# Kernel tuning notes

Hardware: AMD Instinct MI355X
Metric: run time of the kernel (lower is better)

The kernel has to match this reference:

```python
import jax, jax.numpy as jnp
import numpy as np
import math

N, E = 8192, 32768
MUL_S, MUL_V = 32, 16          # 32x0e + 16x1o
DIM = MUL_S + 3 * MUL_V        # 80
NUM_RBF, HID = 16, 64
CUTOFF = 5.0
ALPHA = 5.0 / CUTOFF
# per-edge TP weight sizes (uvw paths): ss->s, s sh1->v, v sh0->v, vv->s, vv->v
O1 = MUL_S * MUL_S              # 1024
O2 = O1 + MUL_S * MUL_V         # 1536
O3 = O2 + MUL_V * MUL_V         # 1792
O4 = O3 + MUL_V * MUL_S         # 2304
WNUM = O4 + MUL_V * MUL_V       # 2560


def setup_inputs() -> dict:
    key = jax.random.key(0)
    ks = jax.random.split(key, 8)
    h = jax.random.normal(ks[0], (N, DIM), jnp.float32)
    pos = jax.random.normal(ks[1], (N, 3), jnp.float32)
    edge_index = jax.random.randint(ks[2], (2, E), 0, N)
    start = math.exp(-CUTOFF)
    means = jnp.linspace(start, 1.0, NUM_RBF).astype(jnp.float32)
    betas = jnp.full((NUM_RBF,), (2.0 / NUM_RBF * (1.0 - start)) ** -2, jnp.float32)
    W1 = jax.random.normal(ks[3], (NUM_RBF, HID), jnp.float32) / np.sqrt(NUM_RBF).astype(np.float32)
    b1 = jnp.zeros((HID,), jnp.float32)
    W2 = jax.random.normal(ks[4], (HID, WNUM), jnp.float32) / np.sqrt(HID).astype(np.float32)
    b2 = jnp.zeros((WNUM,), jnp.float32)
    Wss = jax.random.normal(ks[5], (MUL_S, MUL_S), jnp.float32)
    Wvv = jax.random.normal(ks[6], (MUL_V, MUL_V), jnp.float32)
    return {"h": h, "pos": pos, "edge_index": edge_index, "means": means,
            "betas": betas, "W1": W1, "b1": b1, "W2": W2, "b2": b2,
            "Wss": Wss, "Wvv": Wvv}


def reference(h, pos, edge_index, means, betas, W1, b1, W2, b2, Wss, Wvv):
    src, dst = edge_index[0], edge_index[1]
    vec = pos[dst] - pos[src]                           # [E,3]
    d = jnp.sqrt(jnp.sum(vec * vec, -1) + 1e-12)        # [E]
    y1 = math.sqrt(3.0) * vec / d[:, None]              # l=1 SH, component norm
    # ExpNormalSmearing with cosine cutoff
    cut = 0.5 * (jnp.cos(d * math.pi / CUTOFF) + 1.0) * (d < CUTOFF).astype(h.dtype)
    expd = jnp.exp(-ALPHA * d)[:, None]
    rbf = jnp.exp(-betas * (expd - means) ** 2) * cut[:, None]   # [E,NUM_RBF]
    # edge MLP -> per-edge TP weights
    ew = jax.nn.silu(rbf @ W1 + b1) @ W2 + b2            # [E,WNUM]
    w_ss = ew[:, :O1].reshape(E, MUL_S, MUL_S)
    w_sv = ew[:, O1:O2].reshape(E, MUL_S, MUL_V)
    w_vs = ew[:, O2:O3].reshape(E, MUL_V, MUL_V)
    w_vv0 = ew[:, O3:O4].reshape(E, MUL_V, MUL_S)
    w_vv1 = ew[:, O4:].reshape(E, MUL_V, MUL_V)
    hs = h[:, :MUL_S]                                    # [N,32]
    hv = h[:, MUL_S:].reshape(N, MUL_V, 3)               # [N,16,3]
    s_src = hs[src]                                      # [E,32]
    v_src = hv[src]                                      # [E,16,3]
    # scalar outputs: (0e x 0e -> 0e) + (1o x 1o -> 0e)
    p1 = jnp.einsum('eu,euw->ew', s_src, w_ss)
    dot = jnp.einsum('eud,ed->eu', v_src, y1) / math.sqrt(3.0)
    p4 = jnp.einsum('eu,euw->ew', dot, w_vv0)
    out_s = (p1 / math.sqrt(MUL_S) + p4 / math.sqrt(MUL_V)) / math.sqrt(2.0)
    # vector outputs: (0e x 1o -> 1o) + (1o x 0e -> 1o) + (1o x 1o -> 1o)
    p2 = jnp.einsum('eu,euw,ed->ewd', s_src, w_sv, y1)
    p3 = jnp.einsum('eud,euw->ewd', v_src, w_vs)
    cross = jnp.cross(v_src, y1[:, None, :]) / math.sqrt(2.0)
    p5 = jnp.einsum('eud,euw->ewd', cross, w_vv1)
    out_v = (p2 / math.sqrt(MUL_S) + p3 / math.sqrt(MUL_V) + p5 / math.sqrt(MUL_V)) / math.sqrt(3.0)
    msgs = jnp.concatenate([out_s, out_v.reshape(E, 3 * MUL_V)], -1)   # [E,80]
    # scatter-mean to destination nodes
    agg = jax.ops.segment_sum(msgs, dst, num_segments=N)
    cnt = jax.ops.segment_sum(jnp.ones((E,), msgs.dtype), dst, num_segments=N)
    agg = agg / jnp.maximum(cnt, 1.0)[:, None]
    # equivariant self-interaction (per-irrep channel mixing)
    si_s = hs @ Wss / math.sqrt(MUL_S)
    si_v = jnp.einsum('nud,uw->nwd', hv, Wvv) / math.sqrt(MUL_V)
    self_i = jnp.concatenate([si_s, si_v.reshape(N, 3 * MUL_V)], -1)
    return agg + self_i + h   # residual
```

## Files before the change

kernel.cpp:

```cpp
#include <hip/hip_runtime.h>
#include <math.h>

#define NN 8192
#define EE 32768
#define WN 2560
#define EW_STRIDE 260
#define HID_STRIDE 72

typedef unsigned short u16;
typedef unsigned int u32;
typedef short short8 __attribute__((ext_vector_type(8)));
typedef float f32x4 __attribute__((ext_vector_type(4)));

__device__ __forceinline__ u16 f2b(float f) {
    u32 x = __float_as_uint(f);
    return (u16)((x + 0x7fffu + ((x >> 16) & 1u)) >> 16);
}

__global__ __launch_bounds__(256) void w2_transpose(const float* __restrict__ W2,
                                                    u16* __restrict__ W2T) {
    __shared__ float tile[64][65];
    const int c0 = blockIdx.x << 6;
    const int t = threadIdx.x;
    const int tl = t & 63, th = t >> 6;
    #pragma unroll
    for (int r = 0; r < 16; ++r) {
        int k = (r << 2) + th;
        tile[k][tl] = W2[k * WN + c0 + tl];
    }
    __syncthreads();
    #pragma unroll
    for (int r = 0; r < 16; ++r) {
        int c = (r << 2) + th;
        W2T[(size_t)(c0 + c) * 64 + tl] = f2b(tile[tl][c]);
    }
}

__global__ __launch_bounds__(256, 2) void edge_kernel(
    const float* __restrict__ h, const float* __restrict__ pos, const int* __restrict__ ei,
    const float* __restrict__ means, const float* __restrict__ betas,
    const float* __restrict__ W1, const float* __restrict__ b1,
    const u16* __restrict__ W2T, const float* __restrict__ b2,
    float* __restrict__ agg, float* __restrict__ cnt)
{
    __shared__ alignas(16) u16 sh_hidb[32 * HID_STRIDE];
    __shared__ float sh_s[32][32];
    __shared__ float sh_dot[32][16];
    __shared__ float sh_v[32][48];
    __shared__ float sh_cross[32][48];
    __shared__ float sh_y1[32][3];
    __shared__ float sh_geo[32][2];
    __shared__ float sh_q2[32][16];
    __shared__ int   sh_src[32];
    __shared__ int   sh_dst[32];
    __shared__ float sh_ew[32 * EW_STRIDE];

    const int t = threadIdx.x;

    if (t < 32) {
        const int eg = (blockIdx.x << 5) + t;
        const int si = ei[eg];
        const int di = ei[EE + eg];
        float ax = pos[si*3+0], ay = pos[si*3+1], az = pos[si*3+2];
        float bx = pos[di*3+0], by = pos[di*3+1], bz = pos[di*3+2];
        float vx = bx-ax, vy = by-ay, vz = bz-az;
        float d = sqrtf(vx*vx + vy*vy + vz*vz + 1e-12f);
        float invd = 1.7320508075688772f / d;
        sh_y1[t][0] = vx*invd; sh_y1[t][1] = vy*invd; sh_y1[t][2] = vz*invd;
        sh_geo[t][0] = expf(-d);
        sh_geo[t][1] = (d < 5.0f) ? 0.5f*(cosf(d*0.6283185307179586f) + 1.0f) : 0.0f;
        sh_src[t] = si; sh_dst[t] = di;
    }
    __syncthreads();

    {
        const int e = t >> 3, r = t & 7;
        const float expd = sh_geo[e][0], cut = sh_geo[e][1];
        float rbf[16];
        #pragma unroll
        for (int k = 0; k < 16; ++k) {
            float td = expd - means[k];
            rbf[k] = expf(-betas[k]*td*td) * cut;
        }
        short8 pk;
        #pragma unroll
        for (int jj = 0; jj < 8; ++jj) {
            int j = (r << 3) + jj;
            float a = b1[j];
            #pragma unroll
            for (int k = 0; k < 16; ++k) a += rbf[k] * W1[(k<<6) + j];
            float s = a / (1.0f + expf(-a));
            pk[jj] = (short)f2b(s);
        }
        *(short8*)&sh_hidb[e*HID_STRIDE + (r<<3)] = pk;

        const int srcn = sh_src[e];
        const float* hrow = h + srcn*80;
        const float y1x = sh_y1[e][0], y1y = sh_y1[e][1], y1z = sh_y1[e][2];
        #pragma unroll
        for (int i = 0; i < 4; ++i) { int u = (r<<2)+i; sh_s[e][u] = hrow[u]; }
        #pragma unroll
        for (int i = 0; i < 2; ++i) {
            int u = (r<<1)+i;
            float v0 = hrow[32+u*3+0];
            float v1 = hrow[32+u*3+1];
            float v2 = hrow[32+u*3+2];
            sh_v[e][u*3+0] = v0; sh_v[e][u*3+1] = v1; sh_v[e][u*3+2] = v2;
            sh_dot[e][u] = (v0*y1x + v1*y1y + v2*y1z) * 0.5773502691896258f;
            sh_cross[e][u*3+0] = (v1*y1z - v2*y1y) * 0.7071067811865476f;
            sh_cross[e][u*3+1] = (v2*y1x - v0*y1z) * 0.7071067811865476f;
            sh_cross[e][u*3+2] = (v0*y1y - v1*y1x) * 0.7071067811865476f;
        }
    }
    __syncthreads();

    const int ln = t & 63, wv = t >> 6;
    const int quad = ln >> 4, lm = ln & 15;
    short8 af[2][2];
    #pragma unroll
    for (int mt = 0; mt < 2; ++mt)
        #pragma unroll
        for (int ks = 0; ks < 2; ++ks)
            af[mt][ks] = *(const short8*)&sh_hidb[(mt*16+lm)*HID_STRIDE + (ks<<5) + (quad<<3)];

    float outs[4] = {0.f,0.f,0.f,0.f};
    float q2r[2]  = {0.f,0.f};
    float outv[6] = {0.f,0.f,0.f,0.f,0.f,0.f};

    for (int ci = 0; ci < 10; ++ci) {
        if (ci) __syncthreads();

        short8 bf[4][2];
        float b2v[4];
        #pragma unroll
        for (int i = 0; i < 4; ++i) {
            const int coll = (((wv<<2)+i)<<4) + lm;
            const int col  = (ci<<8) + coll;
            #pragma unroll
            for (int ks = 0; ks < 2; ++ks)
                bf[i][ks] = *(const short8*)(W2T + (size_t)col*64 + (ks<<5) + (quad<<3));
            b2v[i] = b2[col];
        }
        f32x4 d[4][2];
        #pragma unroll
        for (int i = 0; i < 4; ++i) {
            d[i][0] = (f32x4){0.f,0.f,0.f,0.f};
            d[i][1] = (f32x4){0.f,0.f,0.f,0.f};
            d[i][0] = __builtin_amdgcn_mfma_f32_16x16x32_bf16(af[0][0], bf[i][0], d[i][0], 0,0,0);
            d[i][0] = __builtin_amdgcn_mfma_f32_16x16x32_bf16(af[0][1], bf[i][1], d[i][0], 0,0,0);
            d[i][1] = __builtin_amdgcn_mfma_f32_16x16x32_bf16(af[1][0], bf[i][0], d[i][1], 0,0,0);
            d[i][1] = __builtin_amdgcn_mfma_f32_16x16x32_bf16(af[1][1], bf[i][1], d[i][1], 0,0,0);
        }
        #pragma unroll
        for (int i = 0; i < 4; ++i) {
            const int coll = (((wv<<2)+i)<<4) + lm;
            #pragma unroll
            for (int r = 0; r < 4; ++r) {
                sh_ew[((quad<<2)+r)*EW_STRIDE + coll]    = d[i][0][r] + b2v[i];
                sh_ew[((quad<<2)+r+16)*EW_STRIDE + coll] = d[i][1][r] + b2v[i];
            }
        }
        __syncthreads();

        if (ci < 4) {
            const int ub = ci << 3;
            #pragma unroll
            for (int k = 0; k < 4; ++k) {
                int p = t + (k<<8); int e = p >> 5; int w = p & 31;
                float s = 0.f;
                #pragma unroll
                for (int j = 0; j < 8; ++j) s += sh_s[e][ub+j] * sh_ew[e*EW_STRIDE + (j<<5)+w];
                outs[k] += 0.125f * s;
            }
        } else if (ci < 6) {
            const int ub = (ci-4) << 4;
            #pragma unroll
            for (int k = 0; k < 2; ++k) {
                int q = t + (k<<8); int e = q >> 4; int w = q & 15;
                float s = 0.f;
                #pragma unroll
                for (int j = 0; j < 16; ++j) s += sh_s[e][ub+j] * sh_ew[e*EW_STRIDE + (j<<4)+w];
                q2r[k] += s;
            }
            if (ci == 5) {
                #pragma unroll
                for (int k = 0; k < 2; ++k) { int q = t + (k<<8); sh_q2[q>>4][q&15] = q2r[k]; }
            }
        } else if (ci == 6) {
            #pragma unroll
            for (int k = 0; k < 6; ++k) {
                int p = t + (k<<8); int e = p/48; int m = p - e*48; int w = m/3; int d2 = m - w*3;
                float s = 0.f;
                #pragma unroll
                for (int u = 0; u < 16; ++u) s += sh_v[e][u*3+d2] * sh_ew[e*EW_STRIDE + (u<<4)+w];
                outv[k] += 0.14433756729740643f * s;
            }
        } else if (ci < 9) {
            const int ub = (ci-7) << 3;
            #pragma unroll
            for (int k = 0; k < 4; ++k) {
                int p = t + (k<<8); int e = p >> 5; int w = p & 31;
                float s = 0.f;
                #pragma unroll
                for (int j = 0; j < 8; ++j) s += sh_dot[e][ub+j] * sh_ew[e*EW_STRIDE + (j<<5)+w];
                outs[k] += 0.17677669529663687f * s;
            }
        } else {
            #pragma unroll
            for (int k = 0; k < 6; ++k) {
                int p = t + (k<<8); int e = p/48; int m = p - e*48; int w = m/3; int d2 = m - w*3;
                float s = 0.f;
                #pragma unroll
                for (int u = 0; u < 16; ++u) s += sh_cross[e][u*3+d2] * sh_ew[e*EW_STRIDE + (u<<4)+w];
                outv[k] += 0.14433756729740643f * s;
            }
        }
    }

    #pragma unroll
    for (int k = 0; k < 4; ++k) {
        int p = t + (k<<8); int e = p >> 5; int w = p & 31;
        atomicAdd(&agg[sh_dst[e]*80 + w], outs[k]);
    }
    #pragma unroll
    for (int k = 0; k < 6; ++k) {
        int p = t + (k<<8); int e = p/48; int m = p - e*48; int w = m/3; int d2 = m - w*3;
        float val = outv[k] + sh_q2[e][w]*sh_y1[e][d2]*0.10206207261596574f;
        atomicAdd(&agg[sh_dst[e]*80 + 32 + m], val);
    }
    if (t < 32) atomicAdd(&cnt[sh_dst[t]], 1.0f);
}

__global__ __launch_bounds__(256, 4) void node_kernel(
    const float* __restrict__ h, const float* __restrict__ Wss, const float* __restrict__ Wvv,
    const float* __restrict__ agg, const float* __restrict__ cnt,
    float* __restrict__ out)
{
    const int idx = blockIdx.x*256 + threadIdx.x;
    const int n = idx / 80;
    const int j = idx - n*80;
    float a = agg[idx] / fmaxf(cnt[n], 1.0f);
    const float* hrow = h + n*80;
    float si = 0.f;
    if (j < 32) {
        #pragma unroll
        for (int u = 0; u < 32; ++u) si += hrow[u] * Wss[(u<<5)+j];
        si *= 0.17677669529663687f;
    } else {
        int m = j - 32; int w = m/3; int d = m - w*3;
        #pragma unroll
        for (int u = 0; u < 16; ++u) si += hrow[32+u*3+d] * Wvv[(u<<4)+w];
        si *= 0.25f;
    }
    out[idx] = a + si + hrow[j];
}

extern "C" void kernel_launch(void* const* d_in, const int* in_sizes, int n_in,
                              void* d_out, int out_size, void* d_ws, size_t ws_size,
                              hipStream_t stream) {
    const float* h     = (const float*)d_in[0];
    const float* pos   = (const float*)d_in[1];
    const int*   ei    = (const int*)d_in[2];
    const float* means = (const float*)d_in[3];
    const float* betas = (const float*)d_in[4];
    const float* W1    = (const float*)d_in[5];
    const float* b1    = (const float*)d_in[6];
    const float* W2    = (const float*)d_in[7];
    const float* b2    = (const float*)d_in[8];
    const float* Wss   = (const float*)d_in[9];
    const float* Wvv   = (const float*)d_in[10];

    float* agg = (float*)d_ws;
    float* cnt = agg + (size_t)NN*80;
    u16*   W2T = (u16*)(cnt + NN);

    hipMemsetAsync(d_ws, 0, (size_t)(NN*80 + NN)*sizeof(float), stream);
    hipLaunchKernelGGL(w2_transpose, dim3(WN/64), dim3(256), 0, stream, W2, W2T);
    hipLaunchKernelGGL(edge_kernel, dim3(EE/32), dim3(256), 0, stream,
                       h, pos, ei, means, betas, W1, b1, W2T, b2, agg, cnt);
    hipLaunchKernelGGL(node_kernel, dim3((NN*80)/256), dim3(256), 0, stream,
                       h, Wss, Wvv, agg, cnt, (float*)d_out);
}
```

Measured before the change: 155.6 us.

## Consume MFMA edge-weight outputs in registers and fold memset into prep kernel

The edge MLP output tile is no longer written to a large shared-memory buffer and re-read for each tensor-product path. Each wave now contracts its MFMA accumulator fragments directly against pre-scaled source features and keeps per-lane partial sums in registers. The partial sums from the four waves are reduced through shared memory once at the end. The per-chunk barriers go away and shared memory shrinks, which could allow more resident blocks. The workspace memset and the W2 transpose are also merged into a single prep kernel to save one launch. In exchange the kernel has a larger register footprint, a cross-wave reduction step, and scaling constants that were reworked and need to stay correct.

```diff
diff --git a/kernel.cpp b/kernel.cpp
--- a/kernel.cpp
+++ b/kernel.cpp
@@ -4,7 +4,6 @@
 #define NN 8192
 #define EE 32768
 #define WN 2560
-#define EW_STRIDE 260
 #define HID_STRIDE 72
 
 typedef unsigned short u16;
@@ -17,22 +16,31 @@
     return (u16)((x + 0x7fffu + ((x >> 16) & 1u)) >> 16);
 }
 
-__global__ __launch_bounds__(256) void w2_transpose(const float* __restrict__ W2,
-                                                    u16* __restrict__ W2T) {
-    __shared__ float tile[64][65];
-    const int c0 = blockIdx.x << 6;
-    const int t = threadIdx.x;
-    const int tl = t & 63, th = t >> 6;
-    #pragma unroll
-    for (int r = 0; r < 16; ++r) {
-        int k = (r << 2) + th;
-        tile[k][tl] = W2[k * WN + c0 + tl];
-    }
-    __syncthreads();
-    #pragma unroll
-    for (int r = 0; r < 16; ++r) {
-        int c = (r << 2) + th;
-        W2T[(size_t)(c0 + c) * 64 + tl] = f2b(tile[tl][c]);
+__global__ __launch_bounds__(256) void prep(const float* __restrict__ W2,
+                                            u16* __restrict__ W2T,
+                                            float* __restrict__ zbase) {
+    const int t = threadIdx.x, b = blockIdx.x;
+    const float4 z4 = {0.f, 0.f, 0.f, 0.f};
+    #pragma unroll
+    for (int k = 0; k < 3; ++k) {
+        int i = b * 768 + k * 256 + t;
+        if (i < 165888) ((float4*)zbase)[i] = z4;
+    }
+    if (b < 40) {
+        __shared__ float tile[64][65];
+        const int c0 = b << 6;
+        const int tl = t & 63, th = t >> 6;
+        #pragma unroll
+        for (int r = 0; r < 16; ++r) {
+            int kk = (r << 2) + th;
+            tile[kk][tl] = W2[kk * WN + c0 + tl];
+        }
+        __syncthreads();
+        #pragma unroll
+        for (int r = 0; r < 16; ++r) {
+            int c = (r << 2) + th;
+            W2T[(size_t)(c0 + c) * 64 + tl] = f2b(tile[tl][c]);
+        }
     }
 }
 
@@ -43,17 +51,20 @@
     const u16* __restrict__ W2T, const float* __restrict__ b2,
     float* __restrict__ agg, float* __restrict__ cnt)
 {
-    __shared__ alignas(16) u16 sh_hidb[32 * HID_STRIDE];
-    __shared__ float sh_s[32][32];
-    __shared__ float sh_dot[32][16];
-    __shared__ float sh_v[32][48];
-    __shared__ float sh_cross[32][48];
+    __shared__ alignas(16) char sbuf[50688];
+    float (*sh_ss)[33]    = (float (*)[33])(sbuf);
+    float (*sh_dot)[17]   = (float (*)[17])(sbuf + 4224);
+    float (*sh_v)[68]     = (float (*)[68])(sbuf + 6400);
+    float (*sh_cross)[68] = (float (*)[68])(sbuf + 15104);
+    u16*  sh_hidb         = (u16*)(sbuf + 23808);
+    float (*redS)[32][33] = (float (*)[32][33])(sbuf);
+    float (*redQ)[32][17] = (float (*)[32][17])(sbuf + 16896);
+    float (*redV)[32][49] = (float (*)[32][49])(sbuf + 25600);
+
     __shared__ float sh_y1[32][3];
     __shared__ float sh_geo[32][2];
-    __shared__ float sh_q2[32][16];
     __shared__ int   sh_src[32];
     __shared__ int   sh_dst[32];
-    __shared__ float sh_ew[32 * EW_STRIDE];
 
     const int t = threadIdx.x;
 
@@ -98,18 +109,20 @@
         const float* hrow = h + srcn*80;
         const float y1x = sh_y1[e][0], y1y = sh_y1[e][1], y1z = sh_y1[e][2];
         #pragma unroll
-        for (int i = 0; i < 4; ++i) { int u = (r<<2)+i; sh_s[e][u] = hrow[u]; }
+        for (int i = 0; i < 4; ++i) { int u = (r<<2)+i; sh_ss[e][u] = 0.125f * hrow[u]; }
         #pragma unroll
         for (int i = 0; i < 2; ++i) {
             int u = (r<<1)+i;
             float v0 = hrow[32+u*3+0];
             float v1 = hrow[32+u*3+1];
             float v2 = hrow[32+u*3+2];
-            sh_v[e][u*3+0] = v0; sh_v[e][u*3+1] = v1; sh_v[e][u*3+2] = v2;
-            sh_dot[e][u] = (v0*y1x + v1*y1y + v2*y1z) * 0.5773502691896258f;
-            sh_cross[e][u*3+0] = (v1*y1z - v2*y1y) * 0.7071067811865476f;
-            sh_cross[e][u*3+1] = (v2*y1x - v0*y1z) * 0.7071067811865476f;
-            sh_cross[e][u*3+2] = (v0*y1y - v1*y1x) * 0.7071067811865476f;
+            sh_v[e][(u<<2)+0] = v0 * 0.14433756729740643f;
+            sh_v[e][(u<<2)+1] = v1 * 0.14433756729740643f;
+            sh_v[e][(u<<2)+2] = v2 * 0.14433756729740643f;
+            sh_dot[e][u] = (v0*y1x + v1*y1y + v2*y1z) * 0.10206207261596574f;
+            sh_cross[e][(u<<2)+0] = (v1*y1z - v2*y1y) * 0.10206207261596574f;
+            sh_cross[e][(u<<2)+1] = (v2*y1x - v0*y1z) * 0.10206207261596574f;
+            sh_cross[e][(u<<2)+2] = (v0*y1y - v1*y1x) * 0.10206207261596574f;
         }
     }
     __syncthreads();
@@ -123,22 +136,28 @@
         for (int ks = 0; ks < 2; ++ks)
             af[mt][ks] = *(const short8*)&sh_hidb[(mt*16+lm)*HID_STRIDE + (ks<<5) + (quad<<3)];
 
-    float outs[4] = {0.f,0.f,0.f,0.f};
-    float q2r[2]  = {0.f,0.f};
-    float outv[6] = {0.f,0.f,0.f,0.f,0.f,0.f};
-
+    float accS[2][4][2];
+    float accQ[2][4];
+    float accV[2][4][3];
+    #pragma unroll
+    for (int mt = 0; mt < 2; ++mt)
+        #pragma unroll
+        for (int r = 0; r < 4; ++r) {
+            accS[mt][r][0] = accS[mt][r][1] = 0.f;
+            accQ[mt][r] = 0.f;
+            accV[mt][r][0] = accV[mt][r][1] = accV[mt][r][2] = 0.f;
+        }
+
+    #pragma unroll
     for (int ci = 0; ci < 10; ++ci) {
-        if (ci) __syncthreads();
-
-        short8 bf[4][2];
+        short8 bfr[4][2];
         float b2v[4];
         #pragma unroll
         for (int i = 0; i < 4; ++i) {
             const int coll = (((wv<<2)+i)<<4) + lm;
             const int col  = (ci<<8) + coll;
-            #pragma unroll
-            for (int ks = 0; ks < 2; ++ks)
-                bf[i][ks] = *(const short8*)(W2T + (size_t)col*64 + (ks<<5) + (quad<<3));
+            bfr[i][0] = *(const short8*)(W2T + (size_t)col*64 + (quad<<3));
+            bfr[i][1] = *(const short8*)(W2T + (size_t)col*64 + 32 + (quad<<3));
             b2v[i] = b2[col];
         }
         f32x4 d[4][2];
@@ -146,86 +165,111 @@
         for (int i = 0; i < 4; ++i) {
             d[i][0] = (f32x4){0.f,0.f,0.f,0.f};
             d[i][1] = (f32x4){0.f,0.f,0.f,0.f};
-            d[i][0] = __builtin_amdgcn_mfma_f32_16x16x32_bf16(af[0][0], bf[i][0], d[i][0], 0,0,0);
-            d[i][0] = __builtin_amdgcn_mfma_f32_16x16x32_bf16(af[0][1], bf[i][1], d[i][0], 0,0,0);
-            d[i][1] = __builtin_amdgcn_mfma_f32_16x16x32_bf16(af[1][0], bf[i][0], d[i][1], 0,0,0);
-            d[i][1] = __builtin_amdgcn_mfma_f32_16x16x32_bf16(af[1][1], bf[i][1], d[i][1], 0,0,0);
-        }
-        #pragma unroll
-        for (int i = 0; i < 4; ++i) {
-            const int coll = (((wv<<2)+i)<<4) + lm;
-            #pragma unroll
-            for (int r = 0; r < 4; ++r) {
-                sh_ew[((quad<<2)+r)*EW_STRIDE + coll]    = d[i][0][r] + b2v[i];
-                sh_ew[((quad<<2)+r+16)*EW_STRIDE + coll] = d[i][1][r] + b2v[i];
-            }
-        }
-        __syncthreads();
+            d[i][0] = __builtin_amdgcn_mfma_f32_16x16x32_bf16(af[0][0], bfr[i][0], d[i][0], 0,0,0);
+            d[i][0] = __builtin_amdgcn_mfma_f32_16x16x32_bf16(af[0][1], bfr[i][1], d[i][0], 0,0,0);
+            d[i][1] = __builtin_amdgcn_mfma_f32_16x16x32_bf16(af[1][0], bfr[i][0], d[i][1], 0,0,0);
+            d[i][1] = __builtin_amdgcn_mfma_f32_16x16x32_bf16(af[1][1], bfr[i][1], d[i][1], 0,0,0);
+            d[i][0] += b2v[i];
+            d[i][1] += b2v[i];
+        }
 
         if (ci < 4) {
-            const int ub = ci << 3;
-            #pragma unroll
-            for (int k = 0; k < 4; ++k) {
-                int p = t + (k<<8); int e = p >> 5; int w = p & 31;
-                float s = 0.f;
-                #pragma unroll
-                for (int j = 0; j < 8; ++j) s += sh_s[e][ub+j] * sh_ew[e*EW_STRIDE + (j<<5)+w];
-                outs[k] += 0.125f * s;
-            }
+            const int ub = (ci<<3) + (wv<<1);
+            #pragma unroll
+            for (int mt = 0; mt < 2; ++mt)
+                #pragma unroll
+                for (int r = 0; r < 4; ++r) {
+                    const int e = (mt<<4) + (quad<<2) + r;
+                    float s0 = sh_ss[e][ub], s1 = sh_ss[e][ub+1];
+                    accS[mt][r][0] += s0*d[0][mt][r] + s1*d[2][mt][r];
+                    accS[mt][r][1] += s0*d[1][mt][r] + s1*d[3][mt][r];
+                }
         } else if (ci < 6) {
-            const int ub = (ci-4) << 4;
-            #pragma unroll
-            for (int k = 0; k < 2; ++k) {
-                int q = t + (k<<8); int e = q >> 4; int w = q & 15;
-                float s = 0.f;
-                #pragma unroll
-                for (int j = 0; j < 16; ++j) s += sh_s[e][ub+j] * sh_ew[e*EW_STRIDE + (j<<4)+w];
-                q2r[k] += s;
-            }
-            if (ci == 5) {
-                #pragma unroll
-                for (int k = 0; k < 2; ++k) { int q = t + (k<<8); sh_q2[q>>4][q&15] = q2r[k]; }
-            }
+            const int ub = ((ci-4)<<4) + (wv<<2);
+            #pragma unroll
+            for (int mt = 0; mt < 2; ++mt)
+                #pragma unroll
+                for (int r = 0; r < 4; ++r) {
+                    const int e = (mt<<4) + (quad<<2) + r;
+                    float a = 0.f;
+                    #pragma unroll
+                    for (int i = 0; i < 4; ++i) a += sh_ss[e][ub+i] * d[i][mt][r];
+                    accQ[mt][r] += a;
+                }
         } else if (ci == 6) {
-            #pragma unroll
-            for (int k = 0; k < 6; ++k) {
-                int p = t + (k<<8); int e = p/48; int m = p - e*48; int w = m/3; int d2 = m - w*3;
-                float s = 0.f;
-                #pragma unroll
-                for (int u = 0; u < 16; ++u) s += sh_v[e][u*3+d2] * sh_ew[e*EW_STRIDE + (u<<4)+w];
-                outv[k] += 0.14433756729740643f * s;
-            }
+            const int ub = wv << 2;
+            #pragma unroll
+            for (int mt = 0; mt < 2; ++mt)
+                #pragma unroll
+                for (int r = 0; r < 4; ++r) {
+                    const int e = (mt<<4) + (quad<<2) + r;
+                    #pragma unroll
+                    for (int i = 0; i < 4; ++i) {
+                        const float4 vv = *(const float4*)&sh_v[e][(ub+i)<<2];
+                        float ew = d[i][mt][r];
+                        accV[mt][r][0] += vv.x * ew;
+                        accV[mt][r][1] += vv.y * ew;
+                        accV[mt][r][2] += vv.z * ew;
+                    }
+                }
         } else if (ci < 9) {
-            const int ub = (ci-7) << 3;
-            #pragma unroll
-            for (int k = 0; k < 4; ++k) {
-                int p = t + (k<<8); int e = p >> 5; int w = p & 31;
-                float s = 0.f;
-                #pragma unroll
-                for (int j = 0; j < 8; ++j) s += sh_dot[e][ub+j] * sh_ew[e*EW_STRIDE + (j<<5)+w];
-                outs[k] += 0.17677669529663687f * s;
-            }
+            const int ub = ((ci-7)<<3) + (wv<<1);
+            #pragma unroll
+            for (int mt = 0; mt < 2; ++mt)
+                #pragma unroll
+                for (int r = 0; r < 4; ++r) {
+                    const int e = (mt<<4) + (quad<<2) + r;
+                    float s0 = sh_dot[e][ub], s1 = sh_dot[e][ub+1];
+                    accS[mt][r][0] += s0*d[0][mt][r] + s1*d[2][mt][r];
+                    accS[mt][r][1] += s0*d[1][mt][r] + s1*d[3][mt][r];
+                }
         } else {
-            #pragma unroll
-            for (int k = 0; k < 6; ++k) {
-                int p = t + (k<<8); int e = p/48; int m = p - e*48; int w = m/3; int d2 = m - w*3;
-                float s = 0.f;
-                #pragma unroll
-                for (int u = 0; u < 16; ++u) s += sh_cross[e][u*3+d2] * sh_ew[e*EW_STRIDE + (u<<4)+w];
-                outv[k] += 0.14433756729740643f * s;
-            }
-        }
-    }
+            const int ub = wv << 2;
+            #pragma unroll
+            for (int mt = 0; mt < 2; ++mt)
+                #pragma unroll
+                for (int r = 0; r < 4; ++r) {
+                    const int e = (mt<<4) + (quad<<2) + r;
+                    #pragma unroll
+                    for (int i = 0; i < 4; ++i) {
+                        const float4 cc = *(const float4*)&sh_cross[e][(ub+i)<<2];
+                        float ew = d[i][mt][r];
+                        accV[mt][r][0] += cc.x * ew;
+                        accV[mt][r][1] += cc.y * ew;
+                        accV[mt][r][2] += cc.z * ew;
+                    }
+                }
+        }
+    }
+
+    __syncthreads();
+
+    #pragma unroll
+    for (int mt = 0; mt < 2; ++mt)
+        #pragma unroll
+        for (int r = 0; r < 4; ++r) {
+            const int e = (mt<<4) + (quad<<2) + r;
+            redS[wv][e][lm]      = accS[mt][r][0];
+            redS[wv][e][lm+16]   = accS[mt][r][1];
+            redQ[wv][e][lm]      = accQ[mt][r];
+            redV[wv][e][lm*3+0]  = accV[mt][r][0];
+            redV[wv][e][lm*3+1]  = accV[mt][r][1];
+            redV[wv][e][lm*3+2]  = accV[mt][r][2];
+        }
+    __syncthreads();
 
     #pragma unroll
     for (int k = 0; k < 4; ++k) {
         int p = t + (k<<8); int e = p >> 5; int w = p & 31;
-        atomicAdd(&agg[sh_dst[e]*80 + w], outs[k]);
+        float v = redS[0][e][w] + redS[1][e][w] + redS[2][e][w] + redS[3][e][w];
+        atomicAdd(&agg[sh_dst[e]*80 + w], v);
     }
     #pragma unroll
     for (int k = 0; k < 6; ++k) {
-        int p = t + (k<<8); int e = p/48; int m = p - e*48; int w = m/3; int d2 = m - w*3;
-        float val = outv[k] + sh_q2[e][w]*sh_y1[e][d2]*0.10206207261596574f;
+        int p = t + (k<<8); int e = p/48; int m = p - e*48; int w = m/3; int dd = m - w*3;
+        float pv = redV[0][e][m] + redV[1][e][m] + redV[2][e][m] + redV[3][e][m];
+        float q2 = redQ[0][e][w] + redQ[1][e][w] + redQ[2][e][w] + redQ[3][e][w];
+        float val = pv + q2 * sh_y1[e][dd] * 0.8164965809277261f;
         atomicAdd(&agg[sh_dst[e]*80 + 32 + m], val);
     }
     if (t < 32) atomicAdd(&cnt[sh_dst[t]], 1.0f);
@@ -274,8 +318,7 @@
     float* cnt = agg + (size_t)NN*80;
     u16*   W2T = (u16*)(cnt + NN);
 
-    hipMemsetAsync(d_ws, 0, (size_t)(NN*80 + NN)*sizeof(float), stream);
-    hipLaunchKernelGGL(w2_transpose, dim3(WN/64), dim3(256), 0, stream, W2, W2T);
+    hipLaunchKernelGGL(prep, dim3(256), dim3(256), 0, stream, W2, W2T, agg);
     hipLaunchKernelGGL(edge_kernel, dim3(EE/32), dim3(256), 0, stream,
                        h, pos, ei, means, betas, W1, b1, W2T, b2, agg, cnt);
     hipLaunchKernelGGL(node_kernel, dim3((NN*80)/256), dim3(256), 0, stream,
```

New measurement: 141.9 us. 8.8% less time.
